# Kernel tuning notes

Measured on AMD Instinct MI355X. Metric: run time of the kernel, lower is better.

## Reference

```python
import jax, jax.numpy as jnp
import numpy as np
from jax import lax

IN_DIM, OUT_DIM, GROUPS, K, DEGREE, PAD = 64, 128, 4, 3, 3, 1
IN_G = IN_DIM // GROUPS    # 16
OUT_G = OUT_DIM // GROUPS  # 32
EPS = 1e-5


def setup_inputs() -> dict:
    key = jax.random.key(0)
    k1, k2 = jax.random.split(key)
    x = jax.random.normal(k1, (64, IN_DIM, 64, 64), jnp.float32)
    # meta (hypernetwork-generated) weight: (out_g, in_g*(degree+2), k, k)
    layer_weight = jax.random.normal(k2, (OUT_G, IN_G * (DEGREE + 2), K, K), jnp.float32) * 0.05
    return {"x": x, "layer_weight": layer_weight}


def _conv(x, w):
    # plain NCHW conv2d, groups=1, stride=1, dilation=1, symmetric padding
    return lax.conv_general_dilated(
        x, w, window_strides=(1, 1), padding=[(PAD, PAD), (PAD, PAD)],
        dimension_numbers=("NCHW", "OIHW", "NCHW"))


def _legendre_basis(x, order):
    # recursive Legendre polynomials P0..P_order, concatenated on channel dim
    polys = [jnp.ones_like(x), x]
    for n in range(1, order):
        pn = ((2.0 * n + 1.0) * x * polys[-1] - n * polys[-2]) / (n + 1.0)
        polys.append(pn)
    return jnp.concatenate(polys, axis=1)  # [B, in_g*(order+1), H, W]


def _group_forward(xg, w):
    # xg: [B, in_g, H, W]; w: [out_g, in_g*(degree+2), k, k]
    base_w = w[:, :IN_G]                                   # (out_g, in_g, k, k)
    base_out = _conv(jax.nn.silu(xg), base_w)
    # global min-max normalization over the whole group tensor
    xmin, xmax = xg.min(), xg.max()
    x_norm = 2.0 * (xg - xmin) / (xmax - xmin) - 1.0
    lb = _legendre_basis(x_norm, DEGREE)                   # [B, in_g*(degree+1), H, W]
    poly_w = w[:, IN_G:].reshape(OUT_G, IN_G * (DEGREE + 1), K, K)
    y = base_out + _conv(lb, poly_w)
    # InstanceNorm2d (affine=False, no running stats): per-sample per-channel
    mean = y.mean(axis=(2, 3), keepdims=True)
    var = y.var(axis=(2, 3), keepdims=True)
    y = (y - mean) * lax.rsqrt(var + EPS)
    return jax.nn.silu(y)


def reference(x, layer_weight):
    B, C, H, W = x.shape
    # split channels into groups, vmap over groups (same weight for each group)
    xg = x.reshape(B, GROUPS, IN_G, H, W).transpose(1, 0, 2, 3, 4)  # [G,B,in_g,H,W]
    yg = jax.vmap(lambda xx: _group_forward(xx, layer_weight))(xg)  # [G,B,out_g,H,W]
    return yg.transpose(1, 0, 2, 3, 4).reshape(B, OUT_DIM, H, W)
```

## Files before the change

### kernel.cpp

```cpp
#include <hip/hip_runtime.h>
#include <hip/hip_bf16.h>


#define NB 64
#define NH 64
#define NW 64

typedef __attribute__((ext_vector_type(8)))  short bf16x8;
typedef __attribute__((ext_vector_type(8)))  unsigned short u16x8;
typedef __attribute__((ext_vector_type(16))) float f32x16;

__device__ __forceinline__ float silu(float v) {
    return v / (1.0f + __expf(-v));
}
__device__ __forceinline__ unsigned short tobf(float f) {
    union { __hip_bfloat16 h; unsigned short u; } cv;
    cv.h = __float2bfloat16(f);
    return cv.u;
}

__global__ __launch_bounds__(256) void minmax_kernel(const float* __restrict__ x,
                                                     float* __restrict__ pmm) {
    int plane = blockIdx.x;
    const float4* p = (const float4*)(x + (size_t)plane * 4096);
    int t = threadIdx.x;
    float mn = 3.4e38f, mx = -3.4e38f;
    #pragma unroll
    for (int k = 0; k < 4; ++k) {
        float4 v = p[t + k * 256];
        mn = fminf(mn, fminf(fminf(v.x, v.y), fminf(v.z, v.w)));
        mx = fmaxf(mx, fmaxf(fmaxf(v.x, v.y), fmaxf(v.z, v.w)));
    }
    #pragma unroll
    for (int off = 32; off; off >>= 1) {
        mn = fminf(mn, __shfl_xor(mn, off));
        mx = fmaxf(mx, __shfl_xor(mx, off));
    }
    __shared__ float smn[4], smx[4];
    int wid = t >> 6, lane = t & 63;
    if (lane == 0) { smn[wid] = mn; smx[wid] = mx; }
    __syncthreads();
    if (t == 0) {
        mn = fminf(fminf(smn[0], smn[1]), fminf(smn[2], smn[3]));
        mx = fmaxf(fmaxf(smx[0], smx[1]), fmaxf(smx[2], smx[3]));
        pmm[plane * 2]     = mn;
        pmm[plane * 2 + 1] = mx;
    }
}

__global__ __launch_bounds__(256) void reduce_repack_kernel(const float* __restrict__ pmm,
                                                            const float* __restrict__ w,
                                                            float* __restrict__ wsf,
                                                            unsigned short* __restrict__ wpk,
                                                            float* __restrict__ Tt) {
    int blk = blockIdx.x;
    int t = threadIdx.x;
    if (blk < 4) {
        int g = blk;
        float mn = 3.4e38f, mx = -3.4e38f;
        #pragma unroll
        for (int j = 0; j < 4; ++j) {
            int p = t + j * 256;
            int b = p >> 4, c = p & 15;
            int plane = b * 64 + g * 16 + c;
            mn = fminf(mn, pmm[plane * 2]);
            mx = fmaxf(mx, pmm[plane * 2 + 1]);
        }
        #pragma unroll
        for (int off = 32; off; off >>= 1) {
            mn = fminf(mn, __shfl_xor(mn, off));
            mx = fmaxf(mx, __shfl_xor(mx, off));
        }
        __shared__ float smn[4], smx[4];
        int wid = t >> 6, lane = t & 63;
        if (lane == 0) { smn[wid] = mn; smx[wid] = mx; }
        __syncthreads();
        if (t == 0) {
            mn = fminf(fminf(smn[0], smn[1]), fminf(smn[2], smn[3]));
            mx = fmaxf(fmaxf(smx[0], smx[1]), fmaxf(smx[2], smx[3]));
            wsf[g * 2]     = mn;
            wsf[g * 2 + 1] = mx;
        }
    } else if (blk < 76) {
        int idx = (blk - 4) * 256 + t;
        int p   = idx / 4608;
        int r1  = idx - p * 4608;
        int tap = r1 / 512;
        int r2  = r1 - tap * 512;
        int h   = r2 >> 8;
        int oc  = (r2 >> 3) & 31;
        int j   = r2 & 7;
        int k   = p * 16 + h * 8 + j;
        int orig = (k < 16) ? k : (k + 16);
        wpk[idx] = tobf(w[oc * 720 + orig * 9 + tap]);
    } else {
        for (int i = t; i < 288; i += 256) {
            int oc = i / 9, ty = i - oc * 9;
            int ey = ty / 3, ex = ty - ey * 3;
            int ky0 = (ey == 0) ? 1 : 0, ky1 = (ey == 2) ? 1 : 2;
            int kx0 = (ex == 0) ? 1 : 0, kx1 = (ex == 2) ? 1 : 2;
            float s = 0.f;
            for (int c = 0; c < 16; ++c)
                for (int ky = ky0; ky <= ky1; ++ky)
                    for (int kx = kx0; kx <= kx1; ++kx)
                        s += w[oc * 720 + (16 + c) * 9 + ky * 3 + kx];
            Tt[i] = s;
        }
    }
}

__global__ __launch_bounds__(512, 4) void conv_mfma_kernel(const float* __restrict__ x,
                                                           const float* __restrict__ wsf,
                                                           const unsigned short* __restrict__ wpk,
                                                           const float* __restrict__ Tt,
                                                           float* __restrict__ out,
                                                           unsigned short* __restrict__ yscr) {
    __shared__ unsigned short wl[18432];
    __shared__ unsigned short augp[9792];
    __shared__ float Tl[288];

    int flat = blockIdx.x;
    int f = ((flat & 7) << 8) | (flat >> 3);
    int q = f & 7;
    int bg = f >> 3;
    int b = bg & 63;
    int g = bg >> 6;
    int th0 = (q >> 1) * 16, tw0 = (q & 1) * 32;

    float xmin = wsf[g * 2];
    float xmax = wsf[g * 2 + 1];
    float inv = 2.0f / (xmax - xmin);

    const float* xg = x + ((size_t)b * 64 + g * 16) * 4096;
    int t = threadIdx.x;

    {
        const uint4* srcw = (const uint4*)wpk;
        uint4* dstw = (uint4*)wl;
        #pragma unroll
        for (int i = 0; i < 5; ++i) {
            int idx = t + i * 512;
            if (idx < 2304) dstw[idx] = srcw[idx];
        }
    }
    if (t < 288) Tl[t] = Tt[t];

    float r[3][8];
    bool okv[3];
    #pragma unroll
    for (int i = 0; i < 3; ++i) {
        okv[i] = false;
        int idx = t + i * 512;
        if (idx < 1224) {
            int half = idx >= 612 ? 1 : 0;
            int pix = idx - half * 612;
            int ly = pix / 34, lx = pix - ly * 34;
            int gh = th0 + ly - 1, gw = tw0 + lx - 1;
            bool ok = (gh >= 0 && gh < NH && gw >= 0 && gw < NW);
            okv[i] = ok;
            const float* s = xg + (size_t)(half * 8) * 4096 + gh * 64 + gw;
            #pragma unroll
            for (int j = 0; j < 8; ++j)
                r[i][j] = ok ? s[(size_t)j * 4096] : 0.f;
        }
    }

    int wv = t >> 6;
    int lane = t & 63;
    int lo = lane & 31, hi = lane >> 5;
    int py = 2 * wv + (lo >> 4), px = lo & 15;

    f32x16 acc0 = {}, acc1 = {};

    #pragma unroll
    for (int p = 0; p < 4; ++p) {
        #pragma unroll
        for (int i = 0; i < 3; ++i) {
            int idx = t + i * 512;
            if (idx < 1224) {
                int half = idx >= 612 ? 1 : 0;
                int pix = idx - half * 612;
                bf16x8 v;
                #pragma unroll
                for (int j = 0; j < 8; ++j) {
                    float val = r[i][j];
                    float o;
                    if (p == 0) {
                        o = silu(val);
                    } else {
                        float xn = (val - xmin) * inv - 1.f;
                        if (p == 1) o = xn;
                        else {
                            float x2 = xn * xn;
                            o = (p == 2) ? (1.5f * x2 - 0.5f)
                                         : ((2.5f * x2 - 1.5f) * xn);
                        }
                        o = okv[i] ? o : 0.f;
                    }
                    v[j] = (short)tobf(o);
                }
                *(bf16x8*)&augp[(half * 612 + pix) * 8] = v;
            }
        }
        __syncthreads();

        #pragma unroll
        for (int tap = 0; tap < 9; ++tap) {
            const int ky = tap / 3, kx = tap % 3;
            const int hp = (py + ky) * 34 + (px + kx);
            bf16x8 Af = *(const bf16x8*)&wl[(((p * 9 + tap) * 2 + hi) * 32 + lo) * 8];
            bf16x8 Bf0 = *(const bf16x8*)&augp[(hi * 612 + hp) * 8];
            bf16x8 Bf1 = *(const bf16x8*)&augp[(hi * 612 + hp + 16) * 8];
            acc0 = __builtin_amdgcn_mfma_f32_32x32x16_bf16(Af, Bf0, acc0, 0, 0, 0);
            acc1 = __builtin_amdgcn_mfma_f32_32x32x16_bf16(Af, Bf1, acc1, 0, 0, 0);
        }
        __syncthreads();
    }

    int h = th0 + py;
    int ey = (h == 0) ? 0 : ((h == NH - 1) ? 2 : 1);
    size_t gbase = ((size_t)b * 128 + g * 32) * 4096 + (size_t)h * 64;

    int wc0 = tw0 + px;
    int ex0 = (wc0 == 0) ? 0 : ((wc0 == NW - 1) ? 2 : 1);
    int et0 = ey * 3 + ex0;
    int wc1 = tw0 + 16 + px;
    int ex1 = (wc1 == 0) ? 0 : ((wc1 == NW - 1) ? 2 : 1);
    int et1 = ey * 3 + ex1;

    if (yscr) {
        #pragma unroll
        for (int rr = 0; rr < 16; ++rr) {
            int oc = (rr & 3) + 8 * (rr >> 2) + 4 * hi;
            size_t o = gbase + (size_t)oc * 4096;
            yscr[o + wc0] = tobf(acc0[rr] + Tl[oc * 9 + et0]);
            yscr[o + wc1] = tobf(acc1[rr] + Tl[oc * 9 + et1]);
        }
    } else {
        #pragma unroll
        for (int rr = 0; rr < 16; ++rr) {
            int oc = (rr & 3) + 8 * (rr >> 2) + 4 * hi;
            size_t o = gbase + (size_t)oc * 4096;
            out[o + wc0] = acc0[rr] + Tl[oc * 9 + et0];
            out[o + wc1] = acc1[rr] + Tl[oc * 9 + et1];
        }
    }
}

__global__ __launch_bounds__(256) void norm_bf16_kernel(const unsigned short* __restrict__ yscr,
                                                        float* __restrict__ out) {
    int plane = blockIdx.x;
    const u16x8* p = (const u16x8*)(yscr + (size_t)plane * 4096);
    int t = threadIdx.x;
    float v[2][8];
    float s = 0.f, s2 = 0.f;
    #pragma unroll
    for (int k = 0; k < 2; ++k) {
        u16x8 u = p[t + k * 256];
        #pragma unroll
        for (int j = 0; j < 8; ++j) {
            float f = __uint_as_float((unsigned)u[j] << 16);
            v[k][j] = f;
            s += f;
            s2 += f * f;
        }
    }
    #pragma unroll
    for (int off = 32; off; off >>= 1) {
        s  += __shfl_xor(s, off);
        s2 += __shfl_xor(s2, off);
    }
    __shared__ float ss[4], ss2[4];
    int wid = t >> 6, lane = t & 63;
    if (lane == 0) { ss[wid] = s; ss2[wid] = s2; }
    __syncthreads();
    s  = ss[0] + ss[1] + ss[2] + ss[3];
    s2 = ss2[0] + ss2[1] + ss2[2] + ss2[3];
    float mean = s * (1.f / 4096.f);
    float var  = fmaxf(s2 * (1.f / 4096.f) - mean * mean, 0.f);
    float istd = rsqrtf(var + 1e-5f);
    float4* o = (float4*)(out + (size_t)plane * 4096);
    #pragma unroll
    for (int k = 0; k < 2; ++k) {
        float4 a, bq;
        a.x = silu((v[k][0] - mean) * istd);
        a.y = silu((v[k][1] - mean) * istd);
        a.z = silu((v[k][2] - mean) * istd);
        a.w = silu((v[k][3] - mean) * istd);
        bq.x = silu((v[k][4] - mean) * istd);
        bq.y = silu((v[k][5] - mean) * istd);
        bq.z = silu((v[k][6] - mean) * istd);
        bq.w = silu((v[k][7] - mean) * istd);
        o[(t + k * 256) * 2]     = a;
        o[(t + k * 256) * 2 + 1] = bq;
    }
}

__global__ __launch_bounds__(256) void norm_kernel(float* __restrict__ out) {
    int plane = blockIdx.x;
    float4* p = (float4*)(out + (size_t)plane * 4096);
    int t = threadIdx.x;
    float4 v[4];
    float s = 0.f, s2 = 0.f;
    #pragma unroll
    for (int k = 0; k < 4; ++k) {
        v[k] = p[t + k * 256];
        s  += v[k].x + v[k].y + v[k].z + v[k].w;
        s2 += v[k].x * v[k].x + v[k].y * v[k].y + v[k].z * v[k].z + v[k].w * v[k].w;
    }
    #pragma unroll
    for (int off = 32; off; off >>= 1) {
        s  += __shfl_xor(s, off);
        s2 += __shfl_xor(s2, off);
    }
    __shared__ float ss[4], ss2[4];
    int wid = t >> 6, lane = t & 63;
    if (lane == 0) { ss[wid] = s; ss2[wid] = s2; }
    __syncthreads();
    s  = ss[0] + ss[1] + ss[2] + ss[3];
    s2 = ss2[0] + ss2[1] + ss2[2] + ss2[3];
    float mean = s * (1.f / 4096.f);
    float var  = fmaxf(s2 * (1.f / 4096.f) - mean * mean, 0.f);
    float istd = rsqrtf(var + 1e-5f);
    #pragma unroll
    for (int k = 0; k < 4; ++k) {
        float4 o;
        o.x = (v[k].x - mean) * istd; o.x = silu(o.x);
        o.y = (v[k].y - mean) * istd; o.y = silu(o.y);
        o.z = (v[k].z - mean) * istd; o.z = silu(o.z);
        o.w = (v[k].w - mean) * istd; o.w = silu(o.w);
        p[t + k * 256] = o;
    }
}

extern "C" void kernel_launch(void* const* d_in, const int* in_sizes, int n_in,
                              void* d_out, int out_size, void* d_ws, size_t ws_size,
                              hipStream_t stream) {
    const float* x = (const float*)d_in[0];
    const float* w = (const float*)d_in[1];
    float* out = (float*)d_out;
    float* wsf = (float*)d_ws;
    float* pmm = (float*)((char*)d_ws + 64);
    unsigned short* wpk = (unsigned short*)((char*)d_ws + 64 + 32768);
    float* Tt = (float*)((char*)d_ws + 64 + 32768 + 36864);

    const size_t YSCR_OFF = 131072;
    const size_t YSCR_BYTES = (size_t)64 * 128 * 4096 * 2;
    unsigned short* yscr = (ws_size >= YSCR_OFF + YSCR_BYTES)
                         ? (unsigned short*)((char*)d_ws + YSCR_OFF) : nullptr;

    hipLaunchKernelGGL(minmax_kernel, dim3(NB * 64), dim3(256), 0, stream, x, pmm);
    hipLaunchKernelGGL(reduce_repack_kernel, dim3(77), dim3(256), 0, stream, pmm, w, wsf, wpk, Tt);
    hipLaunchKernelGGL(conv_mfma_kernel, dim3(2048), dim3(512), 0, stream, x, wsf, wpk, Tt, out, yscr);
    if (yscr)
        hipLaunchKernelGGL(norm_bf16_kernel, dim3(NB * 128), dim3(256), 0, stream, yscr, out);
    else
        hipLaunchKernelGGL(norm_kernel, dim3(NB * 128), dim3(256), 0, stream, out);
}
```

Before: 129.4 us.

## Widen conv tiles to full rows, cache inputs as bf16, fold repack into minmax

Each conv block now covers a 16x64 full-width tile with four MFMA accumulators instead of a 16x32 tile with two. This halves the number of blocks and the per-block weight staging into LDS, and slightly reduces halo overhead. Staged input pixels are kept in registers as bf16 rather than fp32, so the input is rounded before SiLU and the normalisation, which risks extra accuracy loss. Weight repacking now runs in the same launch as the per-plane min/max pass, and the per-group reduction moves to its own small kernel. LDS use per block grows and register use rises from the extra accumulators.

```diff
diff --git a/kernel.cpp b/kernel.cpp
--- a/kernel.cpp
+++ b/kernel.cpp
@@ -5,6 +5,8 @@
 #define NB 64
 #define NH 64
 #define NW 64
+#define NPIX 1188
+#define NTASK 2376
 
 typedef __attribute__((ext_vector_type(8)))  short bf16x8;
 typedef __attribute__((ext_vector_type(8)))  unsigned short u16x8;
@@ -18,53 +20,26 @@
     cv.h = __float2bfloat16(f);
     return cv.u;
 }
-
-__global__ __launch_bounds__(256) void minmax_kernel(const float* __restrict__ x,
-                                                     float* __restrict__ pmm) {
-    int plane = blockIdx.x;
-    const float4* p = (const float4*)(x + (size_t)plane * 4096);
-    int t = threadIdx.x;
-    float mn = 3.4e38f, mx = -3.4e38f;
-    #pragma unroll
-    for (int k = 0; k < 4; ++k) {
-        float4 v = p[t + k * 256];
-        mn = fminf(mn, fminf(fminf(v.x, v.y), fminf(v.z, v.w)));
-        mx = fmaxf(mx, fmaxf(fmaxf(v.x, v.y), fmaxf(v.z, v.w)));
-    }
-    #pragma unroll
-    for (int off = 32; off; off >>= 1) {
-        mn = fminf(mn, __shfl_xor(mn, off));
-        mx = fmaxf(mx, __shfl_xor(mx, off));
-    }
-    __shared__ float smn[4], smx[4];
-    int wid = t >> 6, lane = t & 63;
-    if (lane == 0) { smn[wid] = mn; smx[wid] = mx; }
-    __syncthreads();
-    if (t == 0) {
-        mn = fminf(fminf(smn[0], smn[1]), fminf(smn[2], smn[3]));
-        mx = fmaxf(fmaxf(smx[0], smx[1]), fmaxf(smx[2], smx[3]));
-        pmm[plane * 2]     = mn;
-        pmm[plane * 2 + 1] = mx;
-    }
-}
-
-__global__ __launch_bounds__(256) void reduce_repack_kernel(const float* __restrict__ pmm,
-                                                            const float* __restrict__ w,
-                                                            float* __restrict__ wsf,
-                                                            unsigned short* __restrict__ wpk,
-                                                            float* __restrict__ Tt) {
+__device__ __forceinline__ float frombf(short u) {
+    return __uint_as_float(((unsigned)(unsigned short)u) << 16);
+}
+
+__global__ __launch_bounds__(256) void prep_kernel(const float* __restrict__ x,
+                                                   const float* __restrict__ w,
+                                                   float* __restrict__ pmm,
+                                                   unsigned short* __restrict__ wpk,
+                                                   float* __restrict__ Tt) {
     int blk = blockIdx.x;
     int t = threadIdx.x;
-    if (blk < 4) {
-        int g = blk;
+    if (blk < 4096) {
+        int plane = blk;
+        const float4* p = (const float4*)(x + (size_t)plane * 4096);
         float mn = 3.4e38f, mx = -3.4e38f;
         #pragma unroll
-        for (int j = 0; j < 4; ++j) {
-            int p = t + j * 256;
-            int b = p >> 4, c = p & 15;
-            int plane = b * 64 + g * 16 + c;
-            mn = fminf(mn, pmm[plane * 2]);
-            mx = fmaxf(mx, pmm[plane * 2 + 1]);
+        for (int k = 0; k < 4; ++k) {
+            float4 v = p[t + k * 256];
+            mn = fminf(mn, fminf(fminf(v.x, v.y), fminf(v.z, v.w)));
+            mx = fmaxf(mx, fmaxf(fmaxf(v.x, v.y), fmaxf(v.z, v.w)));
         }
         #pragma unroll
         for (int off = 32; off; off >>= 1) {
@@ -78,11 +53,11 @@
         if (t == 0) {
             mn = fminf(fminf(smn[0], smn[1]), fminf(smn[2], smn[3]));
             mx = fmaxf(fmaxf(smx[0], smx[1]), fmaxf(smx[2], smx[3]));
-            wsf[g * 2]     = mn;
-            wsf[g * 2 + 1] = mx;
-        }
-    } else if (blk < 76) {
-        int idx = (blk - 4) * 256 + t;
+            pmm[plane * 2]     = mn;
+            pmm[plane * 2 + 1] = mx;
+        }
+    } else if (blk < 4168) {
+        int idx = (blk - 4096) * 256 + t;
         int p   = idx / 4608;
         int r1  = idx - p * 4608;
         int tap = r1 / 512;
@@ -109,6 +84,36 @@
     }
 }
 
+__global__ __launch_bounds__(256) void reduce_kernel(const float* __restrict__ pmm,
+                                                     float* __restrict__ wsf) {
+    int g = blockIdx.x;
+    int t = threadIdx.x;
+    float mn = 3.4e38f, mx = -3.4e38f;
+    #pragma unroll
+    for (int j = 0; j < 4; ++j) {
+        int p = t + j * 256;
+        int b = p >> 4, c = p & 15;
+        int plane = b * 64 + g * 16 + c;
+        mn = fminf(mn, pmm[plane * 2]);
+        mx = fmaxf(mx, pmm[plane * 2 + 1]);
+    }
+    #pragma unroll
+    for (int off = 32; off; off >>= 1) {
+        mn = fminf(mn, __shfl_xor(mn, off));
+        mx = fmaxf(mx, __shfl_xor(mx, off));
+    }
+    __shared__ float smn[4], smx[4];
+    int wid = t >> 6, lane = t & 63;
+    if (lane == 0) { smn[wid] = mn; smx[wid] = mx; }
+    __syncthreads();
+    if (t == 0) {
+        mn = fminf(fminf(smn[0], smn[1]), fminf(smn[2], smn[3]));
+        mx = fmaxf(fmaxf(smx[0], smx[1]), fmaxf(smx[2], smx[3]));
+        wsf[g * 2]     = mn;
+        wsf[g * 2 + 1] = mx;
+    }
+}
+
 __global__ __launch_bounds__(512, 4) void conv_mfma_kernel(const float* __restrict__ x,
                                                            const float* __restrict__ wsf,
                                                            const unsigned short* __restrict__ wpk,
@@ -116,16 +121,16 @@
                                                            float* __restrict__ out,
                                                            unsigned short* __restrict__ yscr) {
     __shared__ unsigned short wl[18432];
-    __shared__ unsigned short augp[9792];
+    __shared__ unsigned short augp[NPIX * 16];
     __shared__ float Tl[288];
 
     int flat = blockIdx.x;
-    int f = ((flat & 7) << 8) | (flat >> 3);
-    int q = f & 7;
-    int bg = f >> 3;
+    int f = ((flat & 7) << 7) | (flat >> 3);
+    int q = f & 3;
+    int bg = f >> 2;
     int b = bg & 63;
     int g = bg >> 6;
-    int th0 = (q >> 1) * 16, tw0 = (q & 1) * 32;
+    int th0 = q * 16;
 
     float xmin = wsf[g * 2];
     float xmax = wsf[g * 2 + 1];
@@ -145,23 +150,22 @@
     }
     if (t < 288) Tl[t] = Tt[t];
 
-    float r[3][8];
-    bool okv[3];
-    #pragma unroll
-    for (int i = 0; i < 3; ++i) {
-        okv[i] = false;
+    bf16x8 rv[5];
+    #pragma unroll
+    for (int i = 0; i < 5; ++i) {
         int idx = t + i * 512;
-        if (idx < 1224) {
-            int half = idx >= 612 ? 1 : 0;
-            int pix = idx - half * 612;
-            int ly = pix / 34, lx = pix - ly * 34;
-            int gh = th0 + ly - 1, gw = tw0 + lx - 1;
+        if (idx < NTASK) {
+            int half = idx >= NPIX ? 1 : 0;
+            int pix = idx - half * NPIX;
+            int ly = pix / 66, lx = pix - ly * 66;
+            int gh = th0 + ly - 1, gw = lx - 1;
             bool ok = (gh >= 0 && gh < NH && gw >= 0 && gw < NW);
-            okv[i] = ok;
             const float* s = xg + (size_t)(half * 8) * 4096 + gh * 64 + gw;
+            bf16x8 v;
             #pragma unroll
             for (int j = 0; j < 8; ++j)
-                r[i][j] = ok ? s[(size_t)j * 4096] : 0.f;
+                v[j] = (short)tobf(ok ? s[(size_t)j * 4096] : 0.f);
+            rv[i] = v;
         }
     }
 
@@ -170,36 +174,40 @@
     int lo = lane & 31, hi = lane >> 5;
     int py = 2 * wv + (lo >> 4), px = lo & 15;
 
-    f32x16 acc0 = {}, acc1 = {};
+    f32x16 acc0 = {}, acc1 = {}, acc2 = {}, acc3 = {};
 
     #pragma unroll
     for (int p = 0; p < 4; ++p) {
         #pragma unroll
-        for (int i = 0; i < 3; ++i) {
+        for (int i = 0; i < 5; ++i) {
             int idx = t + i * 512;
-            if (idx < 1224) {
-                int half = idx >= 612 ? 1 : 0;
-                int pix = idx - half * 612;
-                bf16x8 v;
+            if (idx < NTASK) {
+                int half = idx >= NPIX ? 1 : 0;
+                int pix = idx - half * NPIX;
+                int ly = pix / 66, lx = pix - ly * 66;
+                int gh = th0 + ly - 1, gw = lx - 1;
+                bool ok = (gh >= 0 && gh < NH && gw >= 0 && gw < NW);
+                bf16x8 vv = rv[i];
+                bf16x8 o;
                 #pragma unroll
                 for (int j = 0; j < 8; ++j) {
-                    float val = r[i][j];
-                    float o;
+                    float val = frombf(vv[j]);
+                    float r;
                     if (p == 0) {
-                        o = silu(val);
+                        r = silu(val);
                     } else {
                         float xn = (val - xmin) * inv - 1.f;
-                        if (p == 1) o = xn;
+                        if (p == 1) r = xn;
                         else {
                             float x2 = xn * xn;
-                            o = (p == 2) ? (1.5f * x2 - 0.5f)
+                            r = (p == 2) ? (1.5f * x2 - 0.5f)
                                          : ((2.5f * x2 - 1.5f) * xn);
                         }
-                        o = okv[i] ? o : 0.f;
+                        r = ok ? r : 0.f;
                     }
-                    v[j] = (short)tobf(o);
+                    o[j] = (short)tobf(r);
                 }
-                *(bf16x8*)&augp[(half * 612 + pix) * 8] = v;
+                *(bf16x8*)&augp[(half * NPIX + pix) * 8] = o;
             }
         }
         __syncthreads();
@@ -207,12 +215,16 @@
         #pragma unroll
         for (int tap = 0; tap < 9; ++tap) {
             const int ky = tap / 3, kx = tap % 3;
-            const int hp = (py + ky) * 34 + (px + kx);
+            const int hp = (py + ky) * 66 + (px + kx);
             bf16x8 Af = *(const bf16x8*)&wl[(((p * 9 + tap) * 2 + hi) * 32 + lo) * 8];
-            bf16x8 Bf0 = *(const bf16x8*)&augp[(hi * 612 + hp) * 8];
-            bf16x8 Bf1 = *(const bf16x8*)&augp[(hi * 612 + hp + 16) * 8];
-            acc0 = __builtin_amdgcn_mfma_f32_32x32x16_bf16(Af, Bf0, acc0, 0, 0, 0);
-            acc1 = __builtin_amdgcn_mfma_f32_32x32x16_bf16(Af, Bf1, acc1, 0, 0, 0);
+            bf16x8 B0 = *(const bf16x8*)&augp[(hi * NPIX + hp) * 8];
+            bf16x8 B1 = *(const bf16x8*)&augp[(hi * NPIX + hp + 16) * 8];
+            bf16x8 B2 = *(const bf16x8*)&augp[(hi * NPIX + hp + 32) * 8];
+            bf16x8 B3 = *(const bf16x8*)&augp[(hi * NPIX + hp + 48) * 8];
+            acc0 = __builtin_amdgcn_mfma_f32_32x32x16_bf16(Af, B0, acc0, 0, 0, 0);
+            acc1 = __builtin_amdgcn_mfma_f32_32x32x16_bf16(Af, B1, acc1, 0, 0, 0);
+            acc2 = __builtin_amdgcn_mfma_f32_32x32x16_bf16(Af, B2, acc2, 0, 0, 0);
+            acc3 = __builtin_amdgcn_mfma_f32_32x32x16_bf16(Af, B3, acc3, 0, 0, 0);
         }
         __syncthreads();
     }
@@ -221,12 +233,10 @@
     int ey = (h == 0) ? 0 : ((h == NH - 1) ? 2 : 1);
     size_t gbase = ((size_t)b * 128 + g * 32) * 4096 + (size_t)h * 64;
 
-    int wc0 = tw0 + px;
-    int ex0 = (wc0 == 0) ? 0 : ((wc0 == NW - 1) ? 2 : 1);
-    int et0 = ey * 3 + ex0;
-    int wc1 = tw0 + 16 + px;
-    int ex1 = (wc1 == 0) ? 0 : ((wc1 == NW - 1) ? 2 : 1);
-    int et1 = ey * 3 + ex1;
+    int wc0 = px,      et0 = ey * 3 + ((wc0 == 0) ? 0 : 1);
+    int wc1 = 16 + px, et1 = ey * 3 + 1;
+    int wc2 = 32 + px, et2 = ey * 3 + 1;
+    int wc3 = 48 + px, et3 = ey * 3 + ((wc3 == NW - 1) ? 2 : 1);
 
     if (yscr) {
         #pragma unroll
@@ -235,6 +245,8 @@
             size_t o = gbase + (size_t)oc * 4096;
             yscr[o + wc0] = tobf(acc0[rr] + Tl[oc * 9 + et0]);
             yscr[o + wc1] = tobf(acc1[rr] + Tl[oc * 9 + et1]);
+            yscr[o + wc2] = tobf(acc2[rr] + Tl[oc * 9 + et2]);
+            yscr[o + wc3] = tobf(acc3[rr] + Tl[oc * 9 + et3]);
         }
     } else {
         #pragma unroll
@@ -243,6 +255,8 @@
             size_t o = gbase + (size_t)oc * 4096;
             out[o + wc0] = acc0[rr] + Tl[oc * 9 + et0];
             out[o + wc1] = acc1[rr] + Tl[oc * 9 + et1];
+            out[o + wc2] = acc2[rr] + Tl[oc * 9 + et2];
+            out[o + wc3] = acc3[rr] + Tl[oc * 9 + et3];
         }
     }
 }
@@ -349,9 +363,9 @@
     unsigned short* yscr = (ws_size >= YSCR_OFF + YSCR_BYTES)
                          ? (unsigned short*)((char*)d_ws + YSCR_OFF) : nullptr;
 
-    hipLaunchKernelGGL(minmax_kernel, dim3(NB * 64), dim3(256), 0, stream, x, pmm);
-    hipLaunchKernelGGL(reduce_repack_kernel, dim3(77), dim3(256), 0, stream, pmm, w, wsf, wpk, Tt);
-    hipLaunchKernelGGL(conv_mfma_kernel, dim3(2048), dim3(512), 0, stream, x, wsf, wpk, Tt, out, yscr);
+    hipLaunchKernelGGL(prep_kernel, dim3(4169), dim3(256), 0, stream, x, w, pmm, wpk, Tt);
+    hipLaunchKernelGGL(reduce_kernel, dim3(4), dim3(256), 0, stream, pmm, wsf);
+    hipLaunchKernelGGL(conv_mfma_kernel, dim3(1024), dim3(512), 0, stream, x, wsf, wpk, Tt, out, yscr);
     if (yscr)
         hipLaunchKernelGGL(norm_bf16_kernel, dim3(NB * 128), dim3(256), 0, stream, yscr, out);
     else
```

Result: slower. 168.9 us (+30.5%).
